# Kernel tuning notes

Measured on AMD Instinct MI355X. Metric: run time of the kernel, lower is better.

## Reference

```python
import jax, jax.numpy as jnp
import numpy as np

B_, S_, H_, O_ = 4, 2048, 2048, 2048
E_, R_ = 8, 16
LORA_ALPHA = 16.0


def setup_inputs() -> dict:
    key = jax.random.key(0)
    ks = jax.random.split(key, 5)
    x = jax.random.normal(ks[0], (B_, S_, H_), dtype=jnp.float32)
    W = jax.random.normal(ks[1], (O_, H_), dtype=jnp.float32) * 0.02   # frozen base weight [out, in]
    gate_w = jax.random.normal(ks[2], (E_, H_), dtype=jnp.float32) * 0.02  # router Linear weight [E, H]
    A = jax.random.normal(ks[3], (E_, R_, H_), dtype=jnp.float32) * 0.02   # stacked lora_A weights [E, r, in]
    B = jax.random.normal(ks[4], (E_, O_, R_), dtype=jnp.float32) * 0.02   # stacked lora_B weights [E, out, r]
    return {"x": x, "W": W, "gate_w": gate_w, "A": A, "B": B}


def reference(x, W, gate_w, A, B):
    bsz, seq, hid = x.shape
    E = gate_w.shape[0]
    x_flat = x.reshape(-1, hid)                                  # [T, H]

    # base linear
    out = x_flat @ W.T                                           # [T, O]

    # learned router: softmax -> top-2 -> renormalize
    logits = x_flat @ gate_w.T                                   # [T, E]
    probs = jax.nn.softmax(logits, axis=-1)
    topk_w, topk_idx = jax.lax.top_k(probs, 2)                   # [T, 2]
    topk_w = topk_w / jnp.sum(topk_w, axis=-1, keepdims=True)

    # per-token per-expert combine weight (sum over the 2 slots), scaled by alpha
    onehot = jax.nn.one_hot(topk_idx, E, dtype=x.dtype)          # [T, 2, E]
    wmat = jnp.einsum('tk,tke->te', topk_w, onehot) * LORA_ALPHA # [T, E]

    # dense grouped LoRA: h_e = x A_e^T ; out += sum_e w_te * (h_e B_e^T)
    h = jnp.einsum('th,erh->etr', x_flat, A)                     # [E, T, r]
    hw = h * wmat.T[:, :, None]                                  # [E, T, r]
    lora = jnp.einsum('etr,eor->to', hw, B)                      # [T, O]

    return (out + lora).reshape(bsz, seq, -1)
```

## Files before the change

kernel.cpp:

```cpp
#include <hip/hip_runtime.h>
#include <hip/hip_bf16.h>
#include <stdint.h>

#define T_TOK 8192
#define HID   2048
#define OUTD  2048
#define NE    8
#define RR    16
#define KAUG  2176
#define NH    128
#define NKT   34

typedef __bf16 bf16x8 __attribute__((ext_vector_type(8)));
typedef float  f32x4  __attribute__((ext_vector_type(4)));

#define AS1(p) ((__attribute__((address_space(1))) void*)(p))
#define AS3(p) ((__attribute__((address_space(3))) void*)(p))

__device__ inline unsigned short f2bf(float f) {
  unsigned int u = __builtin_bit_cast(unsigned int, f);
  unsigned int r = (u + 0x7fffu + ((u >> 16) & 1u)) >> 16;
  return (unsigned short)r;
}

__device__ inline ushort4 f2bf4(float4 v) {
  ushort4 u;
  u.x = f2bf(v.x); u.y = f2bf(v.y); u.z = f2bf(v.z); u.w = f2bf(v.w);
  return u;
}

__global__ __launch_bounds__(512) void k_prep(const float* __restrict__ x,
                                              const float* __restrict__ gw,
                                              const float* __restrict__ W,
                                              const float* __restrict__ Bw,
                                              const float* __restrict__ A,
                                              unsigned short* __restrict__ Xa,
                                              float* __restrict__ wte,
                                              unsigned short* __restrict__ Wa,
                                              unsigned short* __restrict__ Ag) {
  __shared__ float gws[NE * HID];
  if (blockIdx.x < 1024) {
#pragma unroll
    for (int i = 0; i < 8; ++i) {
      int idx = (i * 512 + (int)threadIdx.x) * 4;
      *(float4*)(gws + idx) = *(const float4*)(gw + idx);
    }
    __syncthreads();
    int w = threadIdx.x >> 6, lane = threadIdx.x & 63;
    int t = blockIdx.x * 8 + w;
    const float* xt = x + (size_t)t * HID;
    unsigned short* xo = Xa + (size_t)t * KAUG;
    double acc[8] = {0, 0, 0, 0, 0, 0, 0, 0};
#pragma unroll
    for (int i = 0; i < 8; ++i) {
      int k = (i * 64 + lane) * 4;
      float4 xv = *(const float4*)(xt + k);
      *(ushort4*)(xo + k) = f2bf4(xv);
#pragma unroll
      for (int e = 0; e < 8; ++e) {
        float4 gv = *(const float4*)(gws + e * HID + k);
        acc[e] += (double)xv.x * gv.x + (double)xv.y * gv.y +
                  (double)xv.z * gv.z + (double)xv.w * gv.w;
      }
    }
#pragma unroll
    for (int off = 32; off >= 1; off >>= 1)
#pragma unroll
      for (int e = 0; e < 8; ++e)
        acc[e] += __shfl_down(acc[e], off, 64);
    if (lane == 0) {
      int e0 = 0; double l0 = acc[0];
#pragma unroll
      for (int e = 1; e < 8; ++e) if (acc[e] > l0) { l0 = acc[e]; e0 = e; }
      int e1 = -1; double l1 = -1e300;
#pragma unroll
      for (int e = 0; e < 8; ++e) if (e != e0 && acc[e] > l1) { l1 = acc[e]; e1 = e; }
      double w0 = 16.0 / (1.0 + exp(l1 - l0));
      float o[8] = {0.f, 0.f, 0.f, 0.f, 0.f, 0.f, 0.f, 0.f};
      o[e0] = (float)w0;
      o[e1] = (float)(16.0 - w0);
      float4* p = (float4*)(wte + (size_t)t * 8);
      p[0] = make_float4(o[0], o[1], o[2], o[3]);
      p[1] = make_float4(o[4], o[5], o[6], o[7]);
    }
  } else {
    int b2 = blockIdx.x - 1024;
    if (b2 < 2048) {
      int tid = b2 * 512 + threadIdx.x;
      int row = tid >> 9, c = (tid & 511) << 2;
      float4 v = *(const float4*)(W + (size_t)row * HID + c);
      *(ushort4*)(Wa + (size_t)row * KAUG + c) = f2bf4(v);
    } else if (b2 < 2176) {
      int tid = (b2 - 2048) * 512 + threadIdx.x;
      int o = tid >> 5, j = (tid & 31) << 2;
      int e = j >> 4, r = j & 15;
      float4 v = *(const float4*)(Bw + (size_t)e * OUTD * RR + (size_t)o * RR + r);
      *(ushort4*)(Wa + (size_t)o * KAUG + 2048 + j) = f2bf4(v);
    } else {
      int tid = (b2 - 2176) * 512 + threadIdx.x;
      float4 v = *(const float4*)(A + (size_t)tid * 4);
      *(ushort4*)(Ag + (size_t)tid * 4) = f2bf4(v);
    }
  }
}

__global__ __launch_bounds__(256) void k_ha(const unsigned short* __restrict__ Xa,
                                            const unsigned short* __restrict__ Ag,
                                            const float* __restrict__ wte,
                                            unsigned short* __restrict__ XaW) {
  __shared__ unsigned short Xs[4][32 * 64];
  __shared__ unsigned short As[4][64 * 64];
  int tm = (blockIdx.x >> 1) * 32;
  int ch = (blockIdx.x & 1) * 64;
  int w = threadIdx.x >> 6, lane = threadIdx.x & 63;
  int lrow = lane >> 3;
  int lcol_s = (lane & 7) << 3;
  int lcol_g = ((lane & 7) ^ (lrow & 7)) << 3;

  const unsigned short* gX = Xa + (size_t)(tm + w * 8 + lrow) * KAUG + lcol_g;
  const unsigned short* gA = Ag + (size_t)(ch + w * 16 + lrow) * HID + lcol_g;
  int sxo = (w * 8 + lrow) * 64 + lcol_s;
  int sao = (w * 16 + lrow) * 64 + lcol_s;

  f32x4 acc[2] = {};

#define HA_STAGE(slot, koff) do {                                                         \
    __builtin_amdgcn_global_load_lds(AS1(gX + (koff)), AS3(&Xs[slot][0] + sxo), 16, 0, 0);\
    __builtin_amdgcn_global_load_lds(AS1(gA + (koff)), AS3(&As[slot][0] + sao), 16, 0, 0);\
    __builtin_amdgcn_global_load_lds(AS1(gA + (size_t)8 * HID + (koff)),                  \
                                     AS3(&As[slot][0] + 8 * 64 + sao), 16, 0, 0);         \
  } while (0)

#define HA_COMP(s) do {                                                                   \
    _Pragma("unroll")                                                                     \
    for (int ks = 0; ks < 2; ++ks) {                                                      \
      int kch = ks * 4 + (lane >> 4);                                                     \
      int ko = ((kch ^ (lane & 7)) << 3);                                                 \
      bf16x8 a = *(const bf16x8*)(&Xs[s][0] + ((w >> 1) * 16 + (lane & 15)) * 64 + ko);   \
      _Pragma("unroll")                                                                   \
      for (int fn = 0; fn < 2; ++fn) {                                                    \
        bf16x8 bv = *(const bf16x8*)(&As[s][0] + ((w & 1) * 32 + fn * 16 + (lane & 15)) * 64 + ko); \
        acc[fn] = __builtin_amdgcn_mfma_f32_16x16x32_bf16(a, bv, acc[fn], 0, 0, 0);       \
      }                                                                                   \
    }                                                                                     \
  } while (0)

  HA_STAGE(0, 0);
  HA_STAGE(1, 64);
  HA_STAGE(2, 128);
  for (int t = 0; t < 29; ++t) {
    asm volatile("s_waitcnt vmcnt(6)" ::: "memory");
    __builtin_amdgcn_s_barrier();
    HA_COMP(t & 3);
    __builtin_amdgcn_s_barrier();
    HA_STAGE((t + 3) & 3, (t + 3) * 64);
  }
  asm volatile("s_waitcnt vmcnt(6)" ::: "memory");
  __builtin_amdgcn_s_barrier();
  HA_COMP(1);
  asm volatile("s_waitcnt vmcnt(3)" ::: "memory");
  __builtin_amdgcn_s_barrier();
  HA_COMP(2);
  asm volatile("s_waitcnt vmcnt(0)" ::: "memory");
  __builtin_amdgcn_s_barrier();
  HA_COMP(3);
#undef HA_STAGE
#undef HA_COMP

  int q = lane >> 4;
#pragma unroll
  for (int fn = 0; fn < 2; ++fn) {
    int col = ch + (w & 1) * 32 + fn * 16 + (lane & 15);
    int e = col >> 4;
#pragma unroll
    for (int r = 0; r < 4; ++r) {
      int t = tm + (w >> 1) * 16 + q * 4 + r;
      float we = wte[(size_t)t * 8 + e];
      XaW[(size_t)t * KAUG + 2048 + col] = f2bf(we * acc[fn][r]);
    }
  }
}

__global__ __launch_bounds__(512) void k_gemm256(const unsigned short* __restrict__ Xa,
                                                 const unsigned short* __restrict__ Wa,
                                                 float* __restrict__ out) {
  __shared__ unsigned short Asl[2][256 * 64];
  __shared__ unsigned short Bsl[2][256 * 64];
  int bid = blockIdx.x;
  int xcd = bid & 7, idx = bid >> 3;
  int bm = (xcd * 4 + (idx >> 3)) * 256;
  int bn = (idx & 7) * 256;
  int w = threadIdx.x >> 6, lane = threadIdx.x & 63;
  int wm = (w >> 2) * 128;
  int wn = (w & 3) * 64;
  int lrow = lane >> 3;
  int lcol_s = (lane & 7) << 3;
  int lcol_g = ((lane & 7) ^ (lrow & 7)) << 3;

  const unsigned short* gA = Xa + (size_t)(bm + w * 8 + lrow) * KAUG + lcol_g;
  const unsigned short* gB = Wa + (size_t)(bn + w * 8 + lrow) * KAUG + lcol_g;
  int sO = (w * 8 + lrow) * 64 + lcol_s;

#define G_STAGE(p, kt) do {                                                        \
    _Pragma("unroll")                                                              \
    for (int i = 0; i < 4; ++i) {                                                  \
      __builtin_amdgcn_global_load_lds(AS1(gA + (size_t)i * 64 * KAUG + (kt) * 64),\
                                       AS3(&Asl[p][0] + sO + i * 64 * 64), 16, 0, 0); \
      __builtin_amdgcn_global_load_lds(AS1(gB + (size_t)i * 64 * KAUG + (kt) * 64),\
                                       AS3(&Bsl[p][0] + sO + i * 64 * 64), 16, 0, 0); \
    }                                                                              \
  } while (0)

  f32x4 acc[8][4] = {};

#define G_COMP(p) do {                                                             \
    __builtin_amdgcn_s_setprio(1);                                                 \
    _Pragma("unroll")                                                              \
    for (int kk = 0; kk < 2; ++kk) {                                               \
      int kch = kk * 4 + (lane >> 4);                                              \
      int ko = ((kch ^ (lane & 7)) << 3);                                          \
      bf16x8 b[4];                                                                 \
      _Pragma("unroll")                                                            \
      for (int n = 0; n < 4; ++n)                                                  \
        b[n] = *(const bf16x8*)(&Bsl[p][0] + (wn + n * 16 + (lane & 15)) * 64 + ko); \
      _Pragma("unroll")                                                            \
      for (int f = 0; f < 8; ++f) {                                                \
        bf16x8 a = *(const bf16x8*)(&Asl[p][0] + (wm + f * 16 + (lane & 15)) * 64 + ko); \
        _Pragma("unroll")                                                          \
        for (int n = 0; n < 4; ++n)                                                \
          acc[f][n] = __builtin_amdgcn_mfma_f32_16x16x32_bf16(a, b[n], acc[f][n], 0, 0, 0); \
      }                                                                            \
    }                                                                              \
    __builtin_amdgcn_s_setprio(0);                                                 \
  } while (0)

  G_STAGE(0, 0);
  G_STAGE(1, 1);
  for (int kt = 0; kt < 32; kt += 2) {
    asm volatile("s_waitcnt vmcnt(8)" ::: "memory");
    __builtin_amdgcn_s_barrier();
    G_COMP(0);
    __builtin_amdgcn_s_barrier();
    if (kt + 2 < NKT) G_STAGE(0, kt + 2);
    asm volatile("s_waitcnt vmcnt(8)" ::: "memory");
    __builtin_amdgcn_s_barrier();
    G_COMP(1);
    __builtin_amdgcn_s_barrier();
    if (kt + 3 < NKT) G_STAGE(1, kt + 3);
  }
  asm volatile("s_waitcnt vmcnt(8)" ::: "memory");
  __builtin_amdgcn_s_barrier();
  G_COMP(0);
  __builtin_amdgcn_s_barrier();
  asm volatile("s_waitcnt vmcnt(0)" ::: "memory");
  __builtin_amdgcn_s_barrier();
  G_COMP(1);
#undef G_STAGE
#undef G_COMP

#pragma unroll
  for (int f = 0; f < 8; ++f) {
    int row = bm + wm + f * 16 + ((lane >> 4) << 2);
#pragma unroll
    for (int r = 0; r < 4; ++r) {
      float* orow = out + (size_t)(row + r) * OUTD + bn + wn + (lane & 15);
#pragma unroll
      for (int n = 0; n < 4; ++n) orow[n * 16] = acc[f][n][r];
    }
  }
}

extern "C" void kernel_launch(void* const* d_in, const int* in_sizes, int n_in,
                              void* d_out, int out_size, void* d_ws, size_t ws_size,
                              hipStream_t stream) {
  const float* x  = (const float*)d_in[0];
  const float* W  = (const float*)d_in[1];
  const float* gw = (const float*)d_in[2];
  const float* A  = (const float*)d_in[3];
  const float* B  = (const float*)d_in[4];
  float* out = (float*)d_out;

  char* ws = (char*)d_ws;
  unsigned short* Xa  = (unsigned short*)(ws);
  unsigned short* Wa  = (unsigned short*)(ws + 35651584);
  unsigned short* Ag  = (unsigned short*)(ws + 44564480);
  float*          wte = (float*)        (ws + 45088768);

  k_prep   <<<3328, 512, 0, stream>>>(x, gw, W, B, A, Xa, wte, Wa, Ag);
  k_ha     <<<512, 256, 0, stream>>>(Xa, Ag, wte, Xa);
  k_gemm256<<<256, 512, 0, stream>>>(Xa, Wa, out);
}
```

Before: 218.7 us.

## Split GEMM k-tile into four quadrant phases with interleaved half-tile prefetch

Restructures the main bf16 MFMA loop so each 64-wide k-tile is computed in four sub-phases (M-half by N-half). Each phase loads its LDS fragments into registers and issues half of the next tile's global-to-LDS loads, in a style similar to an 8-wave ping-pong schedule. The aim is to spread memory traffic across the compute and hide load latency at finer granularity. In exchange it adds more barriers per tile and relies on fragile vmcnt and buffer-reuse ordering, since it prefetches into the buffer currently being read.

```diff
diff --git a/kernel.cpp b/kernel.cpp
--- a/kernel.cpp
+++ b/kernel.cpp
@@ -201,62 +201,94 @@
   const unsigned short* gB = Wa + (size_t)(bn + w * 8 + lrow) * KAUG + lcol_g;
   int sO = (w * 8 + lrow) * 64 + lcol_s;
 
-#define G_STAGE(p, kt) do {                                                        \
-    _Pragma("unroll")                                                              \
-    for (int i = 0; i < 4; ++i) {                                                  \
-      __builtin_amdgcn_global_load_lds(AS1(gA + (size_t)i * 64 * KAUG + (kt) * 64),\
-                                       AS3(&Asl[p][0] + sO + i * 64 * 64), 16, 0, 0); \
-      __builtin_amdgcn_global_load_lds(AS1(gB + (size_t)i * 64 * KAUG + (kt) * 64),\
-                                       AS3(&Bsl[p][0] + sO + i * 64 * 64), 16, 0, 0); \
-    }                                                                              \
-  } while (0)
-
   f32x4 acc[8][4] = {};
-
-#define G_COMP(p) do {                                                             \
-    __builtin_amdgcn_s_setprio(1);                                                 \
-    _Pragma("unroll")                                                              \
-    for (int kk = 0; kk < 2; ++kk) {                                               \
-      int kch = kk * 4 + (lane >> 4);                                              \
-      int ko = ((kch ^ (lane & 7)) << 3);                                          \
-      bf16x8 b[4];                                                                 \
-      _Pragma("unroll")                                                            \
-      for (int n = 0; n < 4; ++n)                                                  \
-        b[n] = *(const bf16x8*)(&Bsl[p][0] + (wn + n * 16 + (lane & 15)) * 64 + ko); \
-      _Pragma("unroll")                                                            \
-      for (int f = 0; f < 8; ++f) {                                                \
-        bf16x8 a = *(const bf16x8*)(&Asl[p][0] + (wm + f * 16 + (lane & 15)) * 64 + ko); \
-        _Pragma("unroll")                                                          \
-        for (int n = 0; n < 4; ++n)                                                \
-          acc[f][n] = __builtin_amdgcn_mfma_f32_16x16x32_bf16(a, b[n], acc[f][n], 0, 0, 0); \
-      }                                                                            \
-    }                                                                              \
-    __builtin_amdgcn_s_setprio(0);                                                 \
-  } while (0)
-
-  G_STAGE(0, 0);
-  G_STAGE(1, 1);
+  bf16x8 aq[8];
+  bf16x8 bq0[4], bq1[4];
+
+#define STG(arr, gp, p, T, h) do {                                                       \
+    __builtin_amdgcn_global_load_lds(AS1(gp + (size_t)(2*(h)) * 64 * KAUG + (size_t)(T) * 64),   \
+                                     AS3(&arr[p][0] + sO + (2*(h)) * 64 * 64), 16, 0, 0);\
+    __builtin_amdgcn_global_load_lds(AS1(gp + (size_t)(2*(h)+1) * 64 * KAUG + (size_t)(T) * 64), \
+                                     AS3(&arr[p][0] + sO + (2*(h)+1) * 64 * 64), 16, 0, 0);\
+  } while (0)
+
+#define DSR_A(p, MH) do {                                                                \
+    _Pragma("unroll")                                                                    \
+    for (int f = 0; f < 4; ++f)                                                          \
+      _Pragma("unroll")                                                                  \
+      for (int ks = 0; ks < 2; ++ks) {                                                   \
+        int kch = ks * 4 + (lane >> 4);                                                  \
+        int ko = ((kch ^ (lane & 7)) << 3);                                              \
+        aq[f*2+ks] = *(const bf16x8*)(&Asl[p][0] + (wm + (MH)*64 + f*16 + (lane & 15)) * 64 + ko); \
+      }                                                                                  \
+  } while (0)
+
+#define DSR_B(p, NH, bq) do {                                                            \
+    _Pragma("unroll")                                                                    \
+    for (int n = 0; n < 2; ++n)                                                          \
+      _Pragma("unroll")                                                                  \
+      for (int ks = 0; ks < 2; ++ks) {                                                   \
+        int kch = ks * 4 + (lane >> 4);                                                  \
+        int ko = ((kch ^ (lane & 7)) << 3);                                              \
+        bq[n*2+ks] = *(const bf16x8*)(&Bsl[p][0] + (wn + (NH)*32 + n*16 + (lane & 15)) * 64 + ko); \
+      }                                                                                  \
+  } while (0)
+
+#define MM(MH, NH, bq) do {                                                              \
+    __builtin_amdgcn_s_setprio(1);                                                       \
+    _Pragma("unroll")                                                                    \
+    for (int ks = 0; ks < 2; ++ks)                                                       \
+      _Pragma("unroll")                                                                  \
+      for (int f = 0; f < 4; ++f)                                                        \
+        _Pragma("unroll")                                                                \
+        for (int n = 0; n < 2; ++n)                                                      \
+          acc[(MH)*4+f][(NH)*2+n] = __builtin_amdgcn_mfma_f32_16x16x32_bf16(             \
+              aq[f*2+ks], bq[n*2+ks], acc[(MH)*4+f][(NH)*2+n], 0, 0, 0);                 \
+    __builtin_amdgcn_s_setprio(0);                                                       \
+  } while (0)
+
+#define BAR  __builtin_amdgcn_s_barrier()
+#define WLG  asm volatile("s_waitcnt lgkmcnt(0)" ::: "memory")
+
+#define TILE(p, T, S1, S2, S34, VMN) do {                                                \
+                                                                      \
+    DSR_A(p, 0); DSR_B(p, 0, bq0);                                                       \
+    if (S1) STG(Bsl, gB, (p)^1, (T)+1, 1);                                               \
+    BAR; WLG; MM(0, 0, bq0); BAR;                                                        \
+                                                                      \
+    DSR_B(p, 1, bq1);                                                                    \
+    if (S2) STG(Asl, gA, (p)^1, (T)+1, 1);                                               \
+    BAR; WLG; MM(0, 1, bq1); BAR;                                                        \
+                      \
+    DSR_A(p, 1);                                                                         \
+    if (S34) STG(Bsl, gB, (p), (T)+2, 0);                                                \
+    BAR; WLG; MM(1, 0, bq0); BAR;                                                        \
+                      \
+    if (S34) STG(Asl, gA, (p), (T)+2, 0);                                                \
+    asm volatile("s_waitcnt vmcnt(" #VMN ")" ::: "memory");                              \
+    BAR; WLG; MM(1, 1, bq1); BAR;                                                        \
+  } while (0)
+
+  STG(Bsl, gB, 0, 0, 0); STG(Asl, gA, 0, 0, 0);
+  STG(Bsl, gB, 0, 0, 1); STG(Asl, gA, 0, 0, 1);
+  STG(Bsl, gB, 1, 1, 0); STG(Asl, gA, 1, 1, 0);
+  asm volatile("s_waitcnt vmcnt(4)" ::: "memory");
+  BAR;
+
   for (int kt = 0; kt < 32; kt += 2) {
-    asm volatile("s_waitcnt vmcnt(8)" ::: "memory");
-    __builtin_amdgcn_s_barrier();
-    G_COMP(0);
-    __builtin_amdgcn_s_barrier();
-    if (kt + 2 < NKT) G_STAGE(0, kt + 2);
-    asm volatile("s_waitcnt vmcnt(8)" ::: "memory");
-    __builtin_amdgcn_s_barrier();
-    G_COMP(1);
-    __builtin_amdgcn_s_barrier();
-    if (kt + 3 < NKT) G_STAGE(1, kt + 3);
-  }
-  asm volatile("s_waitcnt vmcnt(8)" ::: "memory");
-  __builtin_amdgcn_s_barrier();
-  G_COMP(0);
-  __builtin_amdgcn_s_barrier();
-  asm volatile("s_waitcnt vmcnt(0)" ::: "memory");
-  __builtin_amdgcn_s_barrier();
-  G_COMP(1);
-#undef G_STAGE
-#undef G_COMP
+    TILE(0, kt,     1, 1, 1, 4);
+    TILE(1, kt + 1, 1, 1, 1, 4);
+  }
+  TILE(0, 32, 1, 1, 0, 0);
+  TILE(1, 33, 0, 0, 0, 0);
+
+#undef TILE
+#undef MM
+#undef DSR_A
+#undef DSR_B
+#undef STG
+#undef BAR
+#undef WLG
 
 #pragma unroll
   for (int f = 0; f < 8; ++f) {
```

Result: no change. 219.7 us (+0.5%).
